# Kernel tuning notes

Measured on AMD Instinct MI355X. Metric: run time of the kernel, lower is better.

## Reference

```python
import jax, jax.numpy as jnp
import numpy as np


def _conv1x1(x, w, b):
    # x: [B, Cin, T, H, W], w: [Cout, Cin], b: [Cout] -> [B, Cout, T, H, W]
    return jnp.einsum('bcthw,oc->bothw', x, w) + b[None, :, None, None, None]


def setup_inputs() -> dict:
    key = jax.random.key(0)
    ks = jax.random.split(key, 9)
    B, Ci, T, H, W = 2, 128, 4, 32, 32
    Co = 64
    s_in = 1.0 / np.sqrt(Ci)
    s_out = 1.0 / np.sqrt(Co)
    return {
        'z': jax.random.normal(ks[0], (B, Ci, T, H, W), dtype=jnp.float32),
        'w_theta': jax.random.uniform(ks[1], (Co, Ci), jnp.float32, -s_in, s_in),
        'b_theta': jax.random.uniform(ks[2], (Co,), jnp.float32, -s_in, s_in),
        'w_phi': jax.random.uniform(ks[3], (Co, Ci), jnp.float32, -s_in, s_in),
        'b_phi': jax.random.uniform(ks[4], (Co,), jnp.float32, -s_in, s_in),
        'w_psi': jax.random.uniform(ks[5], (Co, Ci), jnp.float32, -s_in, s_in),
        'b_psi': jax.random.uniform(ks[6], (Co,), jnp.float32, -s_in, s_in),
        'w_v': jax.random.uniform(ks[7], (Ci, Co), jnp.float32, -s_out, s_out),
        'b_v': jax.random.uniform(ks[8], (Ci,), jnp.float32, -s_out, s_out),
    }


def reference(z, w_theta, b_theta, w_phi, b_phi, w_psi, b_psi, w_v, b_v):
    B, Ci, T, H, W = z.shape
    Co = w_theta.shape[0]
    N = T * H * W
    # 1x1 conv projections, flattened to [B, Co, N]
    theta = _conv1x1(z, w_theta, b_theta).reshape(B, Co, N)
    phi = _conv1x1(z, w_phi, b_phi).reshape(B, Co, N)
    psi = _conv1x1(z, w_psi, b_psi).reshape(B, Co, N)
    # g = phi^T @ psi : [B, N, N]; normalize with ReLU(g / N)
    g = jnp.einsum('bcn,bcm->bnm', phi, psi)
    norm_g = jax.nn.relu(g / jnp.asarray(N, z.dtype))
    # tmp = norm_g @ theta^T -> [B, N, Co] -> [B, Co, T, H, W]
    tmp = jnp.einsum('bnm,bcm->bcn', norm_g, theta).reshape(B, Co, T, H, W)
    vg = _conv1x1(tmp, w_v, b_v)
    return vg + z
```

## Files before the change

### kernel.cpp

```cpp
#include <hip/hip_runtime.h>


#define NSEQ 4096
#define CI 128
#define CO 64

typedef __attribute__((ext_vector_type(8))) short bf16x8;
typedef __attribute__((ext_vector_type(4))) short bf16x4;
typedef __attribute__((ext_vector_type(4))) float f32x4;

static __device__ inline short f2bf(float f) {
  union { float f; unsigned u; } v; v.f = f;
  unsigned r = v.u + 0x7fffu + ((v.u >> 16) & 1u);
  return (short)(r >> 16);
}

#define MFMA32(a, b, c) __builtin_amdgcn_mfma_f32_16x16x32_bf16(a, b, c, 0, 0, 0)

#if __has_builtin(__builtin_amdgcn_mfma_f32_16x16x16bf16_1k)
static __device__ inline f32x4 mfma16(bf16x4 a, bf16x4 b, f32x4 c) {
  return __builtin_amdgcn_mfma_f32_16x16x16bf16_1k(a, b, c, 0, 0, 0);
}
#else
static __device__ inline f32x4 mfma16(bf16x4 a, bf16x4 b, f32x4 c) {
  asm("v_mfma_f32_16x16x16_bf16 %0, %1, %2, %0" : "+v"(c) : "v"(a), "v"(b));
  return c;
}
#endif

__global__ __launch_bounds__(256, 1) void proj_kernel(
    const float* __restrict__ z,
    const float* __restrict__ w_th, const float* __restrict__ b_th,
    const float* __restrict__ w_ph, const float* __restrict__ b_ph,
    const float* __restrict__ w_ps, const float* __restrict__ b_ps,
    short* __restrict__ Qg, short* __restrict__ Kg, short* __restrict__ Vt)
{
  __shared__ f32x4 zt4[16384 / 16];
  char* zt = (char*)zt4;

  const int wgid = blockIdx.x;
  const int b = wgid >> 6;
  const int n0 = (wgid & 63) * 64;
  const int t = threadIdx.x;

  {
    const int ck = t & 15;
    const int cr = t >> 4;
#pragma unroll
    for (int g = 0; g < 8; ++g) {
      const int c = g * 16 + cr;
      f32x4 v = *(const f32x4*)(z + (size_t)(b * CI + c) * NSEQ + n0 + ck * 4);
#pragma unroll
      for (int i = 0; i < 4; ++i) {
        const int n = ck * 4 + i;
        const int chunk = (c >> 3) ^ (n & 7);
        *(short*)(zt + n * 256 + chunk * 16 + (c & 7) * 2) = f2bf(v[i]);
      }
    }
  }
  __syncthreads();

  const int w = t >> 6, l = t & 63, lr = l & 15, lg = l >> 4;
  const f32x4 zero4 = {0.f, 0.f, 0.f, 0.f};

  bf16x8 zf[4][4];
#pragma unroll
  for (int nsub = 0; nsub < 4; ++nsub) {
#pragma unroll
    for (int ks = 0; ks < 4; ++ks) {
      const int n = nsub * 16 + lr;
      const int chunk = (ks * 4 + lg) ^ (n & 7);
      zf[nsub][ks] = *(const bf16x8*)(zt + n * 256 + chunk * 16);
    }
  }

  {
    const float* Wm[2]   = {w_ph, w_ps};
    const float* Bm[2]   = {b_ph, b_ps};
    short*       Dm[2]   = {Qg, Kg};
#pragma unroll
    for (int mt = 0; mt < 2; ++mt) {
      bf16x8 wf[4];
#pragma unroll
      for (int ks = 0; ks < 4; ++ks) {
        const float* wp = Wm[mt] + (w * 16 + lr) * CI + ks * 32 + lg * 8;
        f32x4 x0 = *(const f32x4*)wp;
        f32x4 x1 = *(const f32x4*)(wp + 4);
#pragma unroll
        for (int j = 0; j < 4; ++j) { wf[ks][j] = f2bf(x0[j]); wf[ks][4 + j] = f2bf(x1[j]); }
      }
      const f32x4 bias4 = *(const f32x4*)(Bm[mt] + w * 16 + lg * 4);
#pragma unroll
      for (int nsub = 0; nsub < 4; ++nsub) {
        f32x4 acc = zero4;
#pragma unroll
        for (int ks = 0; ks < 4; ++ks)
          acc = MFMA32(wf[ks], zf[nsub][ks], acc);
        bf16x4 pk;
#pragma unroll
        for (int r = 0; r < 4; ++r) pk[r] = f2bf(acc[r] + bias4[r]);
        *(bf16x4*)(Dm[mt] + (size_t)(b * NSEQ + n0 + nsub * 16 + lr) * CO + w * 16 + lg * 4) = pk;
      }
    }
  }

#pragma unroll
  for (int osub = 0; osub < 4; ++osub) {
    f32x4 acc = zero4;
#pragma unroll
    for (int ks = 0; ks < 4; ++ks) {
      const float* wp = w_th + (osub * 16 + lr) * CI + ks * 32 + lg * 8;
      f32x4 x0 = *(const f32x4*)wp;
      f32x4 x1 = *(const f32x4*)(wp + 4);
      bf16x8 wtf;
#pragma unroll
      for (int j = 0; j < 4; ++j) { wtf[j] = f2bf(x0[j]); wtf[4 + j] = f2bf(x1[j]); }
      acc = MFMA32(zf[w][ks], wtf, acc);
    }
    const int o = osub * 16 + lr;
    const float bias = b_th[o];
    bf16x4 pk;
#pragma unroll
    for (int r = 0; r < 4; ++r) pk[r] = f2bf(acc[r] + bias);
    *(bf16x4*)(Vt + (size_t)(b * CO + o) * NSEQ + n0 + w * 16 + lg * 4) = pk;
  }
}

__global__ __launch_bounds__(256, 1) void attn_kernel(
    const short* __restrict__ Qg, const short* __restrict__ Kg,
    const short* __restrict__ Vt, const float* __restrict__ w_v,
    const float* __restrict__ b_v, const float* __restrict__ z,
    float* __restrict__ out)
{
  __shared__ f32x4 smem4[32768 / 16];
  char* smem = (char*)smem4;
  char* Km = smem;
  char* Vm = smem + 16384;

  const int wg = blockIdx.x;
  const int b = wg >> 7;
  const int n0 = (wg & 127) * 32;
  const int t = threadIdx.x;
  const int w = t >> 6, l = t & 63, lr = l & 15, lg = l >> 4;
  const int tw = w >> 1;
  const int nbase = n0 + (w & 1) * 16;
  const f32x4 zero4 = {0.f, 0.f, 0.f, 0.f};

  bf16x8 q0, q1;
  {
    const short* qp = Qg + (size_t)(b * NSEQ + nbase + lr) * CO + lg * 8;
    q0 = *(const bf16x8*)qp;
    q1 = *(const bf16x8*)(qp + 32);
  }

  f32x4 oacc[4];
#pragma unroll
  for (int i = 0; i < 4; ++i) oacc[i] = zero4;

  bf16x8 stg[8];
  auto load_stage = [&](int ss) {
    const int m0 = ss * 128;
#pragma unroll
    for (int r = 0; r < 4; ++r) {
      const int ck = r * 256 + t;
      stg[r] = *(const bf16x8*)(Kg + (size_t)(b * NSEQ + m0 + (ck >> 3)) * CO + (ck & 7) * 8);
    }
#pragma unroll
    for (int r = 0; r < 4; ++r) {
      const int cv = r * 256 + t;
      stg[4 + r] = *(const bf16x8*)(Vt + (size_t)(b * CO + (cv >> 4)) * NSEQ + m0 + (cv & 15) * 8);
    }
  };
  auto write_stage = [&]() {
#pragma unroll
    for (int r = 0; r < 4; ++r) {
      const int ck = r * 256 + t, m = ck >> 3, c8 = ck & 7;
      *(bf16x8*)(Km + m * 128 + ((c8 ^ (m & 7)) * 16)) = stg[r];
    }
#pragma unroll
    for (int r = 0; r < 4; ++r) {
      const int cv = r * 256 + t, o = cv >> 4, mc = cv & 15;
      *(bf16x8*)(Vm + o * 256 + ((mc ^ (o & 7)) * 16)) = stg[4 + r];
    }
  };

  load_stage(0);
  write_stage();
  __syncthreads();

  for (int ss = 0; ss < 32; ++ss) {
    if (ss < 31) load_stage(ss + 1);

#pragma unroll
    for (int msub = 0; msub < 4; ++msub) {
      const int mr = tw * 64 + msub * 16 + lr;
      bf16x8 k0 = *(const bf16x8*)(Km + mr * 128 + ((lg ^ (mr & 7)) * 16));
      bf16x8 k1 = *(const bf16x8*)(Km + mr * 128 + (((4 + lg) ^ (mr & 7)) * 16));
      f32x4 s = MFMA32(k0, q0, zero4);
      s = MFMA32(k1, q1, s);
      bf16x4 pf;
#pragma unroll
      for (int r = 0; r < 4; ++r) {
        const float p = s[r] > 0.f ? s[r] * (1.f / 4096.f) : 0.f;
        pf[r] = f2bf(p);
      }
      const int vchunk = tw * 8 + msub * 2 + (lg >> 1);
      const int voff = (lg & 1) * 8;
#pragma unroll
      for (int osub = 0; osub < 4; ++osub) {
        const int orow = osub * 16 + lr;
        bf16x4 vf = *(const bf16x4*)(Vm + orow * 256 + ((vchunk ^ (orow & 7)) * 16) + voff);
        oacc[osub] = mfma16(vf, pf, oacc[osub]);
      }
    }

    __syncthreads();
    if (ss < 31) {
      write_stage();
      __syncthreads();
    }
  }

  float* red = (float*)smem;
  if (tw == 1) {
    float* dst = red + (w & 1) * 1024;
#pragma unroll
    for (int osub = 0; osub < 4; ++osub)
#pragma unroll
      for (int r = 0; r < 4; ++r)
        dst[(osub * 16 + lg * 4 + r) * 16 + lr] = oacc[osub][r];
  }
  __syncthreads();

  if (tw == 0) {
    const float* sp = red + (w & 1) * 1024;
    bf16x4 of[4];
#pragma unroll
    for (int osub = 0; osub < 4; ++osub) {
#pragma unroll
      for (int r = 0; r < 4; ++r) {
        const float v = oacc[osub][r] + sp[(osub * 16 + lg * 4 + r) * 16 + lr];
        of[osub][r] = f2bf(v);
      }
    }
#pragma unroll
    for (int cis = 0; cis < 8; ++cis) {
      f32x4 e = zero4;
#pragma unroll
      for (int osub = 0; osub < 4; ++osub) {
        f32x4 wl = *(const f32x4*)(w_v + (cis * 16 + lr) * CO + osub * 16 + lg * 4);
        bf16x4 wf;
#pragma unroll
        for (int j = 0; j < 4; ++j) wf[j] = f2bf(wl[j]);
        e = mfma16(wf, of[osub], e);
      }
      const f32x4 bv = *(const f32x4*)(b_v + cis * 16 + lg * 4);
#pragma unroll
      for (int r = 0; r < 4; ++r) {
        const int ci = cis * 16 + lg * 4 + r;
        const size_t off = (size_t)(b * CI + ci) * NSEQ + nbase + lr;
        out[off] = e[r] + z[off] + bv[r];
      }
    }
  }
}

extern "C" void kernel_launch(void* const* d_in, const int* in_sizes, int n_in,
                              void* d_out, int out_size, void* d_ws, size_t ws_size,
                              hipStream_t stream) {
  const float* z    = (const float*)d_in[0];
  const float* w_th = (const float*)d_in[1];
  const float* b_th = (const float*)d_in[2];
  const float* w_ph = (const float*)d_in[3];
  const float* b_ph = (const float*)d_in[4];
  const float* w_ps = (const float*)d_in[5];
  const float* b_ps = (const float*)d_in[6];
  const float* w_v  = (const float*)d_in[7];
  const float* b_v  = (const float*)d_in[8];
  float* out = (float*)d_out;

  short* Qg = (short*)d_ws;
  short* Kg = Qg + 2 * NSEQ * CO;
  short* Vt = Kg + 2 * NSEQ * CO;

  proj_kernel<<<128, 256, 0, stream>>>(z, w_th, b_th, w_ph, b_ph, w_ps, b_ps,
                                       Qg, Kg, Vt);
  attn_kernel<<<256, 256, 0, stream>>>(Qg, Kg, Vt, w_v, b_v, z, out);
}
```

Measured before the change: 125.8 us.

## Split attention over key chunks and add separate reduction/epilogue kernel

```diff
diff --git a/kernel.cpp b/kernel.cpp
--- a/kernel.cpp
+++ b/kernel.cpp
@@ -28,138 +28,112 @@
 }
 #endif
 
-__global__ __launch_bounds__(256, 1) void proj_kernel(
+__global__ __launch_bounds__(256, 2) void proj_kernel(
     const float* __restrict__ z,
     const float* __restrict__ w_th, const float* __restrict__ b_th,
     const float* __restrict__ w_ph, const float* __restrict__ b_ph,
     const float* __restrict__ w_ps, const float* __restrict__ b_ps,
     short* __restrict__ Qg, short* __restrict__ Kg, short* __restrict__ Vt)
 {
-  __shared__ f32x4 zt4[16384 / 16];
-  char* zt = (char*)zt4;
-
-  const int wgid = blockIdx.x;
-  const int b = wgid >> 6;
-  const int n0 = (wgid & 63) * 64;
+  const int bid = blockIdx.x;
+  const int b = bid >> 8;
+  const int n0 = (bid & 255) * 16;
   const int t = threadIdx.x;
-
-  {
-    const int ck = t & 15;
-    const int cr = t >> 4;
-#pragma unroll
-    for (int g = 0; g < 8; ++g) {
-      const int c = g * 16 + cr;
-      f32x4 v = *(const f32x4*)(z + (size_t)(b * CI + c) * NSEQ + n0 + ck * 4);
-#pragma unroll
-      for (int i = 0; i < 4; ++i) {
-        const int n = ck * 4 + i;
-        const int chunk = (c >> 3) ^ (n & 7);
-        *(short*)(zt + n * 256 + chunk * 16 + (c & 7) * 2) = f2bf(v[i]);
-      }
-    }
-  }
-  __syncthreads();
-
   const int w = t >> 6, l = t & 63, lr = l & 15, lg = l >> 4;
   const f32x4 zero4 = {0.f, 0.f, 0.f, 0.f};
 
-  bf16x8 zf[4][4];
-#pragma unroll
-  for (int nsub = 0; nsub < 4; ++nsub) {
-#pragma unroll
-    for (int ks = 0; ks < 4; ++ks) {
-      const int n = nsub * 16 + lr;
-      const int chunk = (ks * 4 + lg) ^ (n & 7);
-      zf[nsub][ks] = *(const bf16x8*)(zt + n * 256 + chunk * 16);
-    }
-  }
-
-  {
-    const float* Wm[2]   = {w_ph, w_ps};
-    const float* Bm[2]   = {b_ph, b_ps};
-    short*       Dm[2]   = {Qg, Kg};
+  bf16x8 zf[4];
+#pragma unroll
+  for (int ks = 0; ks < 4; ++ks) {
+    const float* zp = z + (size_t)(b * CI + ks * 32 + lg * 8) * NSEQ + n0 + lr;
+    float tmp[8];
+#pragma unroll
+    for (int j = 0; j < 8; ++j) tmp[j] = zp[(size_t)j * NSEQ];
+#pragma unroll
+    for (int j = 0; j < 8; ++j) zf[ks][j] = f2bf(tmp[j]);
+  }
+
+  {
+    const float* Wm[2] = {w_ph, w_ps};
+    const float* Bm[2] = {b_ph, b_ps};
+    short*       Dm[2] = {Qg, Kg};
 #pragma unroll
     for (int mt = 0; mt < 2; ++mt) {
-      bf16x8 wf[4];
+      f32x4 acc = zero4;
 #pragma unroll
       for (int ks = 0; ks < 4; ++ks) {
-        const float* wp = Wm[mt] + (w * 16 + lr) * CI + ks * 32 + lg * 8;
+        const float* wp = Wm[mt] + (size_t)(w * 16 + lr) * CI + ks * 32 + lg * 8;
         f32x4 x0 = *(const f32x4*)wp;
         f32x4 x1 = *(const f32x4*)(wp + 4);
-#pragma unroll
-        for (int j = 0; j < 4; ++j) { wf[ks][j] = f2bf(x0[j]); wf[ks][4 + j] = f2bf(x1[j]); }
+        bf16x8 wf;
+#pragma unroll
+        for (int j = 0; j < 4; ++j) { wf[j] = f2bf(x0[j]); wf[4 + j] = f2bf(x1[j]); }
+        acc = MFMA32(wf, zf[ks], acc);
       }
       const f32x4 bias4 = *(const f32x4*)(Bm[mt] + w * 16 + lg * 4);
-#pragma unroll
-      for (int nsub = 0; nsub < 4; ++nsub) {
-        f32x4 acc = zero4;
-#pragma unroll
-        for (int ks = 0; ks < 4; ++ks)
-          acc = MFMA32(wf[ks], zf[nsub][ks], acc);
-        bf16x4 pk;
-#pragma unroll
-        for (int r = 0; r < 4; ++r) pk[r] = f2bf(acc[r] + bias4[r]);
-        *(bf16x4*)(Dm[mt] + (size_t)(b * NSEQ + n0 + nsub * 16 + lr) * CO + w * 16 + lg * 4) = pk;
-      }
-    }
-  }
-
-#pragma unroll
-  for (int osub = 0; osub < 4; ++osub) {
+      bf16x4 pk;
+#pragma unroll
+      for (int r = 0; r < 4; ++r) pk[r] = f2bf(acc[r] + bias4[r]);
+      *(bf16x4*)(Dm[mt] + (size_t)(b * NSEQ + n0 + lr) * CO + w * 16 + lg * 4) = pk;
+    }
+  }
+
+  {
     f32x4 acc = zero4;
 #pragma unroll
     for (int ks = 0; ks < 4; ++ks) {
-      const float* wp = w_th + (osub * 16 + lr) * CI + ks * 32 + lg * 8;
+      const float* wp = w_th + (size_t)(w * 16 + lr) * CI + ks * 32 + lg * 8;
       f32x4 x0 = *(const f32x4*)wp;
       f32x4 x1 = *(const f32x4*)(wp + 4);
       bf16x8 wtf;
 #pragma unroll
       for (int j = 0; j < 4; ++j) { wtf[j] = f2bf(x0[j]); wtf[4 + j] = f2bf(x1[j]); }
-      acc = MFMA32(zf[w][ks], wtf, acc);
-    }
-    const int o = osub * 16 + lr;
-    const float bias = b_th[o];
+      acc = MFMA32(zf[ks], wtf, acc);
+    }
+    const float bias = b_th[w * 16 + lr];
     bf16x4 pk;
 #pragma unroll
     for (int r = 0; r < 4; ++r) pk[r] = f2bf(acc[r] + bias);
-    *(bf16x4*)(Vt + (size_t)(b * CO + o) * NSEQ + n0 + w * 16 + lg * 4) = pk;
-  }
-}
-
-__global__ __launch_bounds__(256, 1) void attn_kernel(
+    *(bf16x4*)(Vt + (size_t)(b * CO + w * 16 + lr) * NSEQ + n0 + lg * 4) = pk;
+  }
+}
+
+__global__ __launch_bounds__(256, 4) void attn_kernel(
     const short* __restrict__ Qg, const short* __restrict__ Kg,
-    const short* __restrict__ Vt, const float* __restrict__ w_v,
-    const float* __restrict__ b_v, const float* __restrict__ z,
-    float* __restrict__ out)
+    const short* __restrict__ Vt, float* __restrict__ Opart)
 {
   __shared__ f32x4 smem4[32768 / 16];
   char* smem = (char*)smem4;
   char* Km = smem;
   char* Vm = smem + 16384;
 
-  const int wg = blockIdx.x;
-  const int b = wg >> 7;
-  const int n0 = (wg & 127) * 32;
+  const int bid = blockIdx.x;
+  const int grp = bid & 7;
+  const int nt = bid >> 3;
+  const int b = grp >> 2, msi = grp & 3;
+  const int n0 = nt * 32;
+  const int m_base = msi * 1024;
   const int t = threadIdx.x;
   const int w = t >> 6, l = t & 63, lr = l & 15, lg = l >> 4;
-  const int tw = w >> 1;
-  const int nbase = n0 + (w & 1) * 16;
   const f32x4 zero4 = {0.f, 0.f, 0.f, 0.f};
 
-  bf16x8 q0, q1;
-  {
-    const short* qp = Qg + (size_t)(b * NSEQ + nbase + lr) * CO + lg * 8;
-    q0 = *(const bf16x8*)qp;
-    q1 = *(const bf16x8*)(qp + 32);
-  }
-
-  f32x4 oacc[4];
-#pragma unroll
-  for (int i = 0; i < 4; ++i) oacc[i] = zero4;
+  bf16x8 q[2][2];
+#pragma unroll
+  for (int nsub = 0; nsub < 2; ++nsub) {
+    const short* qp = Qg + (size_t)(b * NSEQ + n0 + nsub * 16 + lr) * CO + lg * 8;
+    q[nsub][0] = *(const bf16x8*)qp;
+    q[nsub][1] = *(const bf16x8*)(qp + 32);
+  }
+
+  f32x4 oacc[4][2];
+#pragma unroll
+  for (int i = 0; i < 4; ++i)
+#pragma unroll
+    for (int j = 0; j < 2; ++j) oacc[i][j] = zero4;
 
   bf16x8 stg[8];
   auto load_stage = [&](int ss) {
-    const int m0 = ss * 128;
+    const int m0 = m_base + ss * 128;
 #pragma unroll
     for (int r = 0; r < 4; ++r) {
       const int ck = r * 256 + t;
@@ -188,79 +162,122 @@
   write_stage();
   __syncthreads();
 
-  for (int ss = 0; ss < 32; ++ss) {
-    if (ss < 31) load_stage(ss + 1);
-
-#pragma unroll
-    for (int msub = 0; msub < 4; ++msub) {
-      const int mr = tw * 64 + msub * 16 + lr;
+  for (int ss = 0; ss < 8; ++ss) {
+    if (ss < 7) load_stage(ss + 1);
+
+#pragma unroll
+    for (int msub = 0; msub < 2; ++msub) {
+      const int mr = w * 32 + msub * 16 + lr;
       bf16x8 k0 = *(const bf16x8*)(Km + mr * 128 + ((lg ^ (mr & 7)) * 16));
       bf16x8 k1 = *(const bf16x8*)(Km + mr * 128 + (((4 + lg) ^ (mr & 7)) * 16));
-      f32x4 s = MFMA32(k0, q0, zero4);
-      s = MFMA32(k1, q1, s);
-      bf16x4 pf;
-#pragma unroll
-      for (int r = 0; r < 4; ++r) {
-        const float p = s[r] > 0.f ? s[r] * (1.f / 4096.f) : 0.f;
-        pf[r] = f2bf(p);
+      bf16x4 pf[2];
+#pragma unroll
+      for (int nsub = 0; nsub < 2; ++nsub) {
+        f32x4 s = MFMA32(k0, q[nsub][0], zero4);
+        s = MFMA32(k1, q[nsub][1], s);
+#pragma unroll
+        for (int r = 0; r < 4; ++r) {
+          const float p = s[r] > 0.f ? s[r] * (1.f / 4096.f) : 0.f;
+          pf[nsub][r] = f2bf(p);
+        }
       }
-      const int vchunk = tw * 8 + msub * 2 + (lg >> 1);
+      const int vchunk = w * 4 + msub * 2 + (lg >> 1);
       const int voff = (lg & 1) * 8;
 #pragma unroll
       for (int osub = 0; osub < 4; ++osub) {
         const int orow = osub * 16 + lr;
         bf16x4 vf = *(const bf16x4*)(Vm + orow * 256 + ((vchunk ^ (orow & 7)) * 16) + voff);
-        oacc[osub] = mfma16(vf, pf, oacc[osub]);
+        oacc[osub][0] = mfma16(vf, pf[0], oacc[osub][0]);
+        oacc[osub][1] = mfma16(vf, pf[1], oacc[osub][1]);
       }
     }
 
     __syncthreads();
-    if (ss < 31) {
+    if (ss < 7) {
       write_stage();
       __syncthreads();
     }
   }
 
-  float* red = (float*)smem;
-  if (tw == 1) {
-    float* dst = red + (w & 1) * 1024;
+  float* part = (float*)smem;
+  {
+    float* dst = part + w * 2048;
 #pragma unroll
     for (int osub = 0; osub < 4; ++osub)
 #pragma unroll
-      for (int r = 0; r < 4; ++r)
-        dst[(osub * 16 + lg * 4 + r) * 16 + lr] = oacc[osub][r];
+      for (int nsub = 0; nsub < 2; ++nsub)
+#pragma unroll
+        for (int r = 0; r < 4; ++r)
+          dst[(osub * 16 + lg * 4 + r) * 32 + nsub * 16 + lr] = oacc[osub][nsub][r];
   }
   __syncthreads();
-
-  if (tw == 0) {
-    const float* sp = red + (w & 1) * 1024;
-    bf16x4 of[4];
+  {
+    float* gout = Opart + (((size_t)(b * 128 + nt) * 4 + msi) * 2048);
+#pragma unroll
+    for (int pass = 0; pass < 2; ++pass) {
+      const int o = w * 16 + pass * 8 + (l >> 3);
+      const int nq = (l & 7) * 4;
+      f32x4 s = *(const f32x4*)(part + o * 32 + nq);
+#pragma unroll
+      for (int p = 1; p < 4; ++p)
+        s += *(const f32x4*)(part + p * 2048 + o * 32 + nq);
+      *(f32x4*)(gout + o * 32 + nq) = s;
+    }
+  }
+}
+
+__global__ __launch_bounds__(256, 2) void epi_kernel(
+    const float* __restrict__ Opart, const float* __restrict__ w_v,
+    const float* __restrict__ b_v, const float* __restrict__ z,
+    float* __restrict__ out)
+{
+  __shared__ float Olds[64 * 16];
+
+  const int bid = blockIdx.x;
+  const int b = bid >> 8;
+  const int n16 = bid & 255;
+  const int n0 = n16 * 16;
+  const int t = threadIdx.x;
+
+  {
+    const float* src = Opart + ((size_t)(b * 128 + (n16 >> 1)) * 4) * 2048 + (n16 & 1) * 16;
+    const int o = t >> 2, nq = (t & 3) * 4;
+    f32x4 s = *(const f32x4*)(src + o * 32 + nq);
+#pragma unroll
+    for (int p = 1; p < 4; ++p)
+      s += *(const f32x4*)(src + (size_t)p * 2048 + o * 32 + nq);
+    *(f32x4*)(Olds + o * 16 + nq) = s;
+  }
+  __syncthreads();
+
+  const int w = t >> 6, l = t & 63, lr = l & 15, lg = l >> 4;
+  const f32x4 zero4 = {0.f, 0.f, 0.f, 0.f};
+
+  bf16x4 of[4];
+#pragma unroll
+  for (int osub = 0; osub < 4; ++osub)
+#pragma unroll
+    for (int j = 0; j < 4; ++j)
+      of[osub][j] = f2bf(Olds[(osub * 16 + lg * 4 + j) * 16 + lr]);
+
+#pragma unroll
+  for (int c2 = 0; c2 < 2; ++c2) {
+    const int cis = w * 2 + c2;
+    f32x4 e = zero4;
 #pragma unroll
     for (int osub = 0; osub < 4; ++osub) {
-#pragma unroll
-      for (int r = 0; r < 4; ++r) {
-        const float v = oacc[osub][r] + sp[(osub * 16 + lg * 4 + r) * 16 + lr];
-        of[osub][r] = f2bf(v);
-      }
-    }
-#pragma unroll
-    for (int cis = 0; cis < 8; ++cis) {
-      f32x4 e = zero4;
-#pragma unroll
-      for (int osub = 0; osub < 4; ++osub) {
-        f32x4 wl = *(const f32x4*)(w_v + (cis * 16 + lr) * CO + osub * 16 + lg * 4);
-        bf16x4 wf;
-#pragma unroll
-        for (int j = 0; j < 4; ++j) wf[j] = f2bf(wl[j]);
-        e = mfma16(wf, of[osub], e);
-      }
-      const f32x4 bv = *(const f32x4*)(b_v + cis * 16 + lg * 4);
-#pragma unroll
-      for (int r = 0; r < 4; ++r) {
-        const int ci = cis * 16 + lg * 4 + r;
-        const size_t off = (size_t)(b * CI + ci) * NSEQ + nbase + lr;
-        out[off] = e[r] + z[off] + bv[r];
-      }
+      f32x4 wl = *(const f32x4*)(w_v + (size_t)(cis * 16 + lr) * CO + osub * 16 + lg * 4);
+      bf16x4 wf;
+#pragma unroll
+      for (int j = 0; j < 4; ++j) wf[j] = f2bf(wl[j]);
+      e = mfma16(wf, of[osub], e);
+    }
+    const f32x4 bv = *(const f32x4*)(b_v + cis * 16 + lg * 4);
+#pragma unroll
+    for (int r = 0; r < 4; ++r) {
+      const int ci = cis * 16 + lg * 4 + r;
+      const size_t off = (size_t)(b * CI + ci) * NSEQ + n0 + lr;
+      out[off] = e[r] + z[off] + bv[r];
     }
   }
 }
@@ -282,8 +299,10 @@
   short* Qg = (short*)d_ws;
   short* Kg = Qg + 2 * NSEQ * CO;
   short* Vt = Kg + 2 * NSEQ * CO;
-
-  proj_kernel<<<128, 256, 0, stream>>>(z, w_th, b_th, w_ph, b_ph, w_ps, b_ps,
+  float* Opart = (float*)((char*)d_ws + 3u * 1024 * 1024);
+
+  proj_kernel<<<512, 256, 0, stream>>>(z, w_th, b_th, w_ph, b_ph, w_ps, b_ps,
                                        Qg, Kg, Vt);
-  attn_kernel<<<256, 256, 0, stream>>>(Qg, Kg, Vt, w_v, b_v, z, out);
-}
+  attn_kernel<<<1024, 256, 0, stream>>>(Qg, Kg, Vt, Opart);
+  epi_kernel<<<512, 256, 0, stream>>>(Opart, w_v, b_v, z, out);
+}
```

After: 105.8 us. -15.9%, faster.
